# Optimization experiments

Measured on AMD Instinct MI355X. Metric: run time of the kernel, lower is better.

Reference implementation:

```python
import jax, jax.numpy as jnp
import numpy as np

N, E, F_IN, G, C = 100000, 3200000, 64, 1024, 10
BN_EPS = 1e-5


def _glorot(key, shape):
    fan_in, fan_out = shape[0], shape[1]
    lim = jnp.sqrt(6.0 / (fan_in + fan_out))
    return jax.random.uniform(key, shape, jnp.float32, -lim, lim)


def setup_inputs() -> dict:
    key = jax.random.key(0)
    ks = jax.random.split(key, 20)
    x = jax.random.normal(ks[0], (N, F_IN), jnp.float32)
    edge_index = jax.random.randint(ks[1], (2, E), 0, N, jnp.int64)
    batch = jnp.sort(jax.random.randint(ks[2], (N,), 0, G, jnp.int64))
    p = {
        'W1a': _glorot(ks[3], (F_IN, 128)), 'b1a': jnp.zeros((128,), jnp.float32),
        'W1b': _glorot(ks[4], (128, 128)), 'b1b': jnp.zeros((128,), jnp.float32),
        'g1': jnp.ones((128,), jnp.float32), 'be1': jnp.zeros((128,), jnp.float32),
        'W2a': _glorot(ks[5], (128, 64)), 'b2a': jnp.zeros((64,), jnp.float32),
        'W2b': _glorot(ks[6], (64, 64)), 'b2b': jnp.zeros((64,), jnp.float32),
        'g2': jnp.ones((64,), jnp.float32), 'be2': jnp.zeros((64,), jnp.float32),
        'W3a': _glorot(ks[7], (64, 32)), 'b3a': jnp.zeros((32,), jnp.float32),
        'W3b': _glorot(ks[8], (32, 32)), 'b3b': jnp.zeros((32,), jnp.float32),
        'g3': jnp.ones((32,), jnp.float32), 'be3': jnp.zeros((32,), jnp.float32),
        'Wf1': _glorot(ks[9], (32, 128)), 'bf1': jnp.zeros((128,), jnp.float32),
        'Wf2': _glorot(ks[10], (128, 64)), 'bf2': jnp.zeros((64,), jnp.float32),
        'Wf3': _glorot(ks[11], (64, C)), 'bf3': jnp.zeros((C,), jnp.float32),
    }
    return {'x': x, 'edge_index': edge_index, 'batch': batch, **p}


def _gin(x, src, dst, Wa, ba, Wb, bb):
    # GINConv (eps=0): h = MLP(x + sum_{j->i} x_j)
    agg = jax.ops.segment_sum(x[src], dst, num_segments=N)
    h = jax.nn.relu((x + agg) @ Wa + ba)
    return h @ Wb + bb


def _bn(x, g, b):
    # BatchNorm1d, training-mode batch statistics (biased variance)
    mu = jnp.mean(x, axis=0)
    var = jnp.mean((x - mu) ** 2, axis=0)
    return (x - mu) * jax.lax.rsqrt(var + BN_EPS) * g + b


def reference(x, edge_index, batch,
              W1a, b1a, W1b, b1b, g1, be1,
              W2a, b2a, W2b, b2b, g2, be2,
              W3a, b3a, W3b, b3b, g3, be3,
              Wf1, bf1, Wf2, bf2, Wf3, bf3):
    src, dst = edge_index[0], edge_index[1]
    z = _bn(jax.nn.relu(_gin(x, src, dst, W1a, b1a, W1b, b1b)), g1, be1)
    z = _bn(jax.nn.relu(_gin(z, src, dst, W2a, b2a, W2b, b2b)), g2, be2)
    z = _bn(jax.nn.relu(_gin(z, src, dst, W3a, b3a, W3b, b3b)), g3, be3)
    # global_add_pool over graph ids
    z = jax.ops.segment_sum(z, batch, num_segments=G)  # [G, 32]
    cr = jax.nn.relu(z @ Wf1 + bf1)
    cr = jax.nn.relu(cr @ Wf2 + bf2)  # dropout = identity (eval)
    cr = cr @ Wf3 + bf3
    return cr.reshape(-1, C)
```

## Files before the change

### kernel.cpp

```cpp
#include <hip/hip_runtime.h>

#define BN_EPS 1e-5f

typedef _Float16 f16;
typedef _Float16 f16x8 __attribute__((ext_vector_type(8)));
typedef _Float16 f16x4 __attribute__((ext_vector_type(4)));
typedef float f32x4 __attribute__((ext_vector_type(4)));

#define NBLK 512
#define BSHIFT 8
#define BMASK 255

__global__ __launch_bounds__(256) void conv_kernel(const float4* __restrict__ in,
        f16x4* __restrict__ out, int n4) {
    int i = blockIdx.x * 256 + threadIdx.x;
    if (i < n4) {
        float4 v = in[i];
        f16x4 o;
        o.x = (f16)v.x; o.y = (f16)v.y; o.z = (f16)v.z; o.w = (f16)v.w;
        out[i] = o;
    }
}

__global__ __launch_bounds__(256) void bkt_count(const int* __restrict__ dst,
        int* __restrict__ hist, int NBK, int CHUNK, int E) {
    __shared__ int lh[512];
    const int blk = blockIdx.x, t = threadIdx.x;
    for (int r = t; r < 512; r += 256) lh[r] = 0;
    __syncthreads();
    const int e0 = blk * CHUNK, e1 = min(E, e0 + CHUNK);
    for (int e = e0 + t; e < e1; e += 256) atomicAdd(&lh[dst[e] >> BSHIFT], 1);
    __syncthreads();
    for (int r = t; r < NBK; r += 256) hist[r * NBLK + blk] = lh[r];
}

__global__ __launch_bounds__(512) void bkt_bscan(int* __restrict__ hist,
        int* __restrict__ btot) {
    __shared__ int sh[512];
    const int b = blockIdx.x, t = threadIdx.x;
    int v = hist[b * NBLK + t];
    sh[t] = v;
    __syncthreads();
    for (int d = 1; d < 512; d <<= 1) {
        int u = (t >= d) ? sh[t - d] : 0;
        __syncthreads();
        sh[t] += u;
        __syncthreads();
    }
    hist[b * NBLK + t] = sh[t] - v;
    if (t == 511) btot[b] = sh[511];
}

__global__ __launch_bounds__(512) void bkt_boff(const int* __restrict__ btot,
        int* __restrict__ boff, int* __restrict__ off, int NBK, int N, int E) {
    __shared__ int sh[512];
    const int t = threadIdx.x;
    int v = (t < NBK) ? btot[t] : 0;
    sh[t] = v;
    __syncthreads();
    for (int d = 1; d < 512; d <<= 1) {
        int u = (t >= d) ? sh[t - d] : 0;
        __syncthreads();
        sh[t] += u;
        __syncthreads();
    }
    if (t < NBK) boff[t] = sh[t] - v;
    if (t == 0) { boff[NBK] = E; off[N] = E; }
}

__global__ __launch_bounds__(256) void bkt_scatter(const int* __restrict__ src,
        const int* __restrict__ dst, const int* __restrict__ hist,
        const int* __restrict__ boff, int* __restrict__ bucketed,
        int NBK, int CHUNK, int E) {
    __shared__ int lc[512];
    const int blk = blockIdx.x, t = threadIdx.x;
    for (int r = t; r < NBK; r += 256) lc[r] = boff[r] + hist[r * NBLK + blk];
    __syncthreads();
    const int e0 = blk * CHUNK, e1 = min(E, e0 + CHUNK);
    for (int e = e0 + t; e < e1; e += 256) {
        int d = dst[e];
        int slot = atomicAdd(&lc[d >> BSHIFT], 1);
        bucketed[slot] = ((d & BMASK) << 18) | src[e];
    }
}

__global__ __launch_bounds__(512) void bkt_csr(const int* __restrict__ bucketed,
        const int* __restrict__ boff, int* __restrict__ off,
        int* __restrict__ elist, int N) {
    __shared__ int lh[256];
    __shared__ int lc[256];
    __shared__ int sh[256];
    const int b = blockIdx.x, t = threadIdx.x;
    const int b0 = b << BSHIFT;
    const int R = min(N - b0, 256);
    const int base = boff[b], cnt = boff[b + 1] - base;
    if (t < 256) lh[t] = 0;
    __syncthreads();
    for (int i = t; i < cnt; i += 512) atomicAdd(&lh[bucketed[base + i] >> 18], 1);
    __syncthreads();
    int v = 0;
    if (t < 256) { v = lh[t]; sh[t] = v; }
    __syncthreads();
    for (int d = 1; d < 256; d <<= 1) {
        int u = 0;
        if (t < 256 && t >= d) u = sh[t - d];
        __syncthreads();
        if (t < 256) sh[t] += u;
        __syncthreads();
    }
    if (t < 256) { int ex = sh[t] - v; lh[t] = ex; lc[t] = ex; }
    __syncthreads();
    if (t < R) off[b0 + t] = base + lh[t];
    for (int i = t; i < cnt; i += 512) {
        int p = bucketed[base + i];
        int rk = atomicAdd(&lc[p >> 18], 1);
        elist[base + rk] = p & 0x3FFFF;
    }
}

template<int F, bool AFFINE>
__global__ __launch_bounds__(256) void gather_v(const int* __restrict__ off,
        const int* __restrict__ elist, const f16* __restrict__ in,
        f16* __restrict__ out, const float* __restrict__ v,
        const float* __restrict__ bias, int N) {
    constexpr int TPN = F / 8;
    constexpr int NPB = 256 / TPN;
    const int i = blockIdx.x * NPB + threadIdx.x / TPN;
    const int l = threadIdx.x & (TPN - 1);
    if (i >= N) return;
    const int j0 = l * 8;
    f16x8 s = ((const f16x8*)(in + (size_t)i * F))[l];
    float a[8];
#pragma unroll
    for (int u = 0; u < 8; u++) a[u] = (float)s[u];
    int k = off[i], e = off[i + 1];
    const float cnt = (float)(e - k + 1);
    for (; k + 8 <= e; k += 8) {
        f16x8 p0 = ((const f16x8*)(in + (size_t)elist[k + 0] * F))[l];
        f16x8 p1 = ((const f16x8*)(in + (size_t)elist[k + 1] * F))[l];
        f16x8 p2 = ((const f16x8*)(in + (size_t)elist[k + 2] * F))[l];
        f16x8 p3 = ((const f16x8*)(in + (size_t)elist[k + 3] * F))[l];
        f16x8 p4 = ((const f16x8*)(in + (size_t)elist[k + 4] * F))[l];
        f16x8 p5 = ((const f16x8*)(in + (size_t)elist[k + 5] * F))[l];
        f16x8 p6 = ((const f16x8*)(in + (size_t)elist[k + 6] * F))[l];
        f16x8 p7 = ((const f16x8*)(in + (size_t)elist[k + 7] * F))[l];
#pragma unroll
        for (int u = 0; u < 8; u++)
            a[u] += (((float)p0[u] + (float)p1[u]) + ((float)p2[u] + (float)p3[u]))
                  + (((float)p4[u] + (float)p5[u]) + ((float)p6[u] + (float)p7[u]));
    }
    for (; k + 4 <= e; k += 4) {
        f16x8 p0 = ((const f16x8*)(in + (size_t)elist[k + 0] * F))[l];
        f16x8 p1 = ((const f16x8*)(in + (size_t)elist[k + 1] * F))[l];
        f16x8 p2 = ((const f16x8*)(in + (size_t)elist[k + 2] * F))[l];
        f16x8 p3 = ((const f16x8*)(in + (size_t)elist[k + 3] * F))[l];
#pragma unroll
        for (int u = 0; u < 8; u++)
            a[u] += ((float)p0[u] + (float)p1[u]) + ((float)p2[u] + (float)p3[u]);
    }
    for (; k < e; k++) {
        f16x8 p = ((const f16x8*)(in + (size_t)elist[k] * F))[l];
#pragma unroll
        for (int u = 0; u < 8; u++) a[u] += (float)p[u];
    }
    if (AFFINE) {
        float4 vv0 = *(const float4*)(v + j0);
        float4 vv1 = *(const float4*)(v + j0 + 4);
        float4 bb0 = *(const float4*)(bias + j0);
        float4 bb1 = *(const float4*)(bias + j0 + 4);
        a[0] = fmaxf(fmaf(cnt, vv0.x, a[0] + bb0.x), 0.0f);
        a[1] = fmaxf(fmaf(cnt, vv0.y, a[1] + bb0.y), 0.0f);
        a[2] = fmaxf(fmaf(cnt, vv0.z, a[2] + bb0.z), 0.0f);
        a[3] = fmaxf(fmaf(cnt, vv0.w, a[3] + bb0.w), 0.0f);
        a[4] = fmaxf(fmaf(cnt, vv1.x, a[4] + bb1.x), 0.0f);
        a[5] = fmaxf(fmaf(cnt, vv1.y, a[5] + bb1.y), 0.0f);
        a[6] = fmaxf(fmaf(cnt, vv1.z, a[6] + bb1.z), 0.0f);
        a[7] = fmaxf(fmaf(cnt, vv1.w, a[7] + bb1.w), 0.0f);
    }
    f16x8 o;
#pragma unroll
    for (int u = 0; u < 8; u++) o[u] = (f16)a[u];
    ((f16x8*)(out + (size_t)i * F))[l] = o;
}

__global__ __launch_bounds__(64) void prep_kernel(const float* __restrict__ W,
        const float* __restrict__ stats, const float* __restrict__ g,
        const float* __restrict__ be, float* __restrict__ v,
        int FIN, int FOUT, float invN) {
    int j = threadIdx.x;
    if (j >= FOUT) return;
    float acc = 0.0f;
    for (int k = 0; k < FIN; k++) {
        float mu = stats[k] * invN;
        float var = fmaxf(stats[FIN + k] * invN - mu * mu, 0.0f);
        float sc = rsqrtf(var + BN_EPS) * g[k];
        float sh = be[k] - mu * sc;
        acc = fmaf(sh, W[(size_t)k * FOUT + j], acc);
    }
    v[j] = acc;
}

__global__ __launch_bounds__(256) void wfrag_kernel(const float* __restrict__ W,
        f16* __restrict__ out, int FIN, int FOUT,
        const float* __restrict__ stats, const float* __restrict__ g, float invN) {
    int f = blockIdx.x * 256 + threadIdx.x;
    if (f >= FIN * FOUT) return;
    int j = f & 7;
    int lane = (f >> 3) & 63;
    int tile = f >> 9;
    int NT = FOUT >> 4;
    int t = tile % NT, s = tile / NT;
    int k = s * 32 + (lane >> 4) * 8 + j;
    int n = t * 16 + (lane & 15);
    float w = W[(size_t)k * FOUT + n];
    if (stats) {
        float mu = stats[k] * invN;
        float var = fmaxf(stats[FIN + k] * invN - mu * mu, 0.0f);
        w *= rsqrtf(var + BN_EPS) * g[k];
    }
    out[f] = (f16)w;
}

template<int FIN, int FOUT, bool STATS, bool RELU, bool BIAS, typename OutT>
__global__ __launch_bounds__(256) void gemm_mfma(const f16* __restrict__ A,
        const f16* __restrict__ Wf, const float* __restrict__ bias,
        OutT* __restrict__ Out, float* __restrict__ stats, int N) {
    constexpr int NS = FIN / 32;
    constexpr int NT = FOUT / 16;
    __shared__ float Ss[STATS ? 2 * FOUT : 1];
    if (STATS) {
        for (int i = threadIdx.x; i < 2 * FOUT; i += 256) Ss[i] = 0.0f;
        __syncthreads();
    }
    const int wid = threadIdx.x >> 6;
    const int lane = threadIdx.x & 63;
    const int col = lane & 15;
    const int quad = lane >> 4;

    f16x8 Bf[NS][NT];
#pragma unroll
    for (int s = 0; s < NS; s++)
#pragma unroll
        for (int t = 0; t < NT; t++)
            Bf[s][t] = *(const f16x8*)&Wf[((s * NT + t) << 9) + (lane << 3)];

    float bj[NT];
#pragma unroll
    for (int t = 0; t < NT; t++) bj[t] = BIAS ? bias[t * 16 + col] : 0.0f;

    float ls[NT], ls2[NT];
#pragma unroll
    for (int t = 0; t < NT; t++) { ls[t] = 0.0f; ls2[t] = 0.0f; }

    const int S = N >> 4;
    for (int sidx = blockIdx.x * 4 + wid; sidx < S; sidx += (int)gridDim.x * 4) {
        const int m0 = sidx << 4;
        const f16* a0 = A + (size_t)(m0 + col) * FIN + (quad << 3);
        f16x8 Af[NS];
#pragma unroll
        for (int s = 0; s < NS; s++) Af[s] = *(const f16x8*)(a0 + s * 32);
        f32x4 acc[NT];
#pragma unroll
        for (int t = 0; t < NT; t++) acc[t] = (f32x4){bj[t], bj[t], bj[t], bj[t]};
#pragma unroll
        for (int t = 0; t < NT; t++)
#pragma unroll
            for (int s = 0; s < NS; s++)
                acc[t] = __builtin_amdgcn_mfma_f32_16x16x32_f16(Af[s], Bf[s][t], acc[t], 0, 0, 0);
#pragma unroll
        for (int t = 0; t < NT; t++) {
            float v0 = acc[t][0], v1 = acc[t][1], v2 = acc[t][2], v3 = acc[t][3];
            if (RELU) {
                v0 = fmaxf(v0, 0.0f); v1 = fmaxf(v1, 0.0f);
                v2 = fmaxf(v2, 0.0f); v3 = fmaxf(v3, 0.0f);
            }
            if (STATS) {
                ls[t]  += (v0 + v1) + (v2 + v3);
                ls2[t] += (v0 * v0 + v1 * v1) + (v2 * v2 + v3 * v3);
            }
            OutT* o = Out + (size_t)(m0 + quad * 4) * FOUT + t * 16 + col;
            o[0]        = (OutT)v0;
            o[FOUT]     = (OutT)v1;
            o[2 * FOUT] = (OutT)v2;
            o[3 * FOUT] = (OutT)v3;
        }
    }

    if (STATS) {
#pragma unroll
        for (int t = 0; t < NT; t++) {
            float s1 = ls[t], s2 = ls2[t];
            s1 += __shfl_xor(s1, 16); s1 += __shfl_xor(s1, 32);
            s2 += __shfl_xor(s2, 16); s2 += __shfl_xor(s2, 32);
            if (quad == 0) {
                atomicAdd(&Ss[t * 16 + col], s1);
                atomicAdd(&Ss[FOUT + t * 16 + col], s2);
            }
        }
        __syncthreads();
        for (int i = threadIdx.x; i < 2 * FOUT; i += 256) atomicAdd(&stats[i], Ss[i]);
    }
}

__global__ __launch_bounds__(256) void bn_pool_kernel(const float* __restrict__ y,
        const float* __restrict__ stats, const float* __restrict__ gw,
        const float* __restrict__ bw, const int* __restrict__ batch,
        float* __restrict__ pool, int N, float invN) {
    constexpr int F = 32, CH = 64;
    int q = threadIdx.x >> 5;
    int j = threadIdx.x & 31;
    int r0 = (blockIdx.x * 8 + q) * CH;
    if (r0 >= N) return;
    int r1 = min(r0 + CH, N);
    float mu = stats[j] * invN;
    float var = fmaxf(stats[F + j] * invN - mu * mu, 0.0f);
    float sc = rsqrtf(var + BN_EPS) * gw[j];
    float sh = bw[j] - mu * sc;
    int curg = batch[r0];
    float acc = 0.0f;
    for (int r = r0; r < r1; r++) {
        int g = batch[r];
        if (g != curg) {
            atomicAdd(pool + (size_t)curg * 32 + j, acc);
            acc = 0.0f;
            curg = g;
        }
        acc = fmaf(y[(size_t)r * 32 + j], sc, sh + acc);
    }
    atomicAdd(pool + (size_t)curg * 32 + j, acc);
}

__global__ __launch_bounds__(128) void fc_kernel(const float* __restrict__ pool,
        const float* __restrict__ Wf1, const float* __restrict__ bf1,
        const float* __restrict__ Wf2, const float* __restrict__ bf2,
        const float* __restrict__ Wf3, const float* __restrict__ bf3,
        float* __restrict__ out) {
    __shared__ float zin[32];
    __shared__ float h1[128];
    __shared__ float h2[64];
    const int gidx = blockIdx.x;
    const int t = threadIdx.x;
    if (t < 32) zin[t] = pool[(size_t)gidx * 32 + t];
    __syncthreads();
    {
        float a = bf1[t];
        for (int k = 0; k < 32; k++) a = fmaf(zin[k], Wf1[k * 128 + t], a);
        h1[t] = fmaxf(a, 0.0f);
    }
    __syncthreads();
    if (t < 64) {
        float a = bf2[t];
        for (int k = 0; k < 128; k++) a = fmaf(h1[k], Wf2[k * 64 + t], a);
        h2[t] = fmaxf(a, 0.0f);
    }
    __syncthreads();
    if (t < 10) {
        float a = bf3[t];
        for (int k = 0; k < 64; k++) a = fmaf(h2[k], Wf3[k * 10 + t], a);
        out[(size_t)gidx * 10 + t] = a;
    }
}

extern "C" void kernel_launch(void* const* d_in, const int* in_sizes, int n_in,
                              void* d_out, int out_size, void* d_ws, size_t ws_size,
                              hipStream_t stream) {
    const float* x   = (const float*)d_in[0];
    const int*  ei   = (const int*)d_in[1];
    const int*  batch= (const int*)d_in[2];
    const float* W1a = (const float*)d_in[3];  const float* b1a = (const float*)d_in[4];
    const float* W1b = (const float*)d_in[5];  const float* b1b = (const float*)d_in[6];
    const float* g1  = (const float*)d_in[7];  const float* be1 = (const float*)d_in[8];
    const float* W2a = (const float*)d_in[9];  const float* b2a = (const float*)d_in[10];
    const float* W2b = (const float*)d_in[11]; const float* b2b = (const float*)d_in[12];
    const float* g2  = (const float*)d_in[13]; const float* be2 = (const float*)d_in[14];
    const float* W3a = (const float*)d_in[15]; const float* b3a = (const float*)d_in[16];
    const float* W3b = (const float*)d_in[17]; const float* b3b = (const float*)d_in[18];
    const float* g3  = (const float*)d_in[19]; const float* be3 = (const float*)d_in[20];
    const float* Wf1 = (const float*)d_in[21]; const float* bf1 = (const float*)d_in[22];
    const float* Wf2 = (const float*)d_in[23]; const float* bf2 = (const float*)d_in[24];
    const float* Wf3 = (const float*)d_in[25]; const float* bf3 = (const float*)d_in[26];

    const int N = in_sizes[2];
    const int E = in_sizes[1] / 2;
    const int G = out_size / 10;
    const int* src = ei;
    const int* dst = ei + E;

    const int NBK = (N + BMASK) >> BSHIFT;
    const int CHUNK = (E + NBLK - 1) / NBLK;

    float* B0   = (float*)d_ws;
    float* B1   = B0 + (size_t)N * 128;
    float* pool = B1 + (size_t)N * 128;
    float* st1  = pool + (size_t)G * 32;
    float* st2  = st1 + 256;
    float* st3  = st2 + 256;
    int* off    = (int*)(st3 + 256);
    int* elist  = off + (N + 1);
    float* v2   = (float*)(elist + E);
    float* v3   = v2 + 64;
    int* boff   = (int*)(v3 + 32);
    int* btot   = boff + (NBK + 1);
    f16* Wh1a   = (f16*)(btot + NBK);
    f16* Wh1b   = Wh1a + 64 * 128;
    f16* Wh2a   = Wh1b + 128 * 128;
    f16* Wh2b   = Wh2a + 128 * 64;
    f16* Wh3a   = Wh2b + 64 * 64;
    f16* Wh3b   = Wh3a + 64 * 32;

    int* bucketed = (int*)B1;
    int* hist     = bucketed + E;

    f16* xh    = (f16*)B0;
    f16* A1    = (f16*)B1;
    f16* H1    = (f16*)B0 + (size_t)N * 64;
    f16* Y1    = (f16*)B1 + (size_t)N * 64;
    f16* Z1    = (f16*)B0;
    f16* H2    = (f16*)B1;
    f16* Y2    = (f16*)B0 + (size_t)N * 64;
    f16* Z2    = (f16*)B0;
    f16* H3    = (f16*)B1;
    float* Y3  = B1 + (size_t)N * 64;

    hipMemsetAsync(pool, 0, ((size_t)G * 32 + 768) * sizeof(float), stream);

    const float invN = 1.0f / (float)N;
    const int GG = 640;

    conv_kernel<<<(N * 16 + 255) / 256, 256, 0, stream>>>((const float4*)x, (f16x4*)xh, N * 16);

    wfrag_kernel<<<32, 256, 0, stream>>>(W1a, Wh1a, 64, 128, nullptr, nullptr, invN);
    wfrag_kernel<<<64, 256, 0, stream>>>(W1b, Wh1b, 128, 128, nullptr, nullptr, invN);
    wfrag_kernel<<<16, 256, 0, stream>>>(W2b, Wh2b, 64, 64, nullptr, nullptr, invN);
    wfrag_kernel<<<4, 256, 0, stream>>>(W3b, Wh3b, 32, 32, nullptr, nullptr, invN);

    bkt_count  <<<NBLK, 256, 0, stream>>>(dst, hist, NBK, CHUNK, E);
    bkt_bscan  <<<NBK, 512, 0, stream>>>(hist, btot);
    bkt_boff   <<<1, 512, 0, stream>>>(btot, boff, off, NBK, N, E);
    bkt_scatter<<<NBLK, 256, 0, stream>>>(src, dst, hist, boff, bucketed, NBK, CHUNK, E);
    bkt_csr    <<<NBK, 512, 0, stream>>>(bucketed, boff, off, elist, N);

    gather_v<64, false><<<(N + 31) / 32, 256, 0, stream>>>(off, elist, xh, A1, nullptr, nullptr, N);
    gemm_mfma<64, 128, false, true, true, f16><<<GG, 256, 0, stream>>>(A1, Wh1a, b1a, H1, nullptr, N);
    gemm_mfma<128, 128, true, true, true, f16><<<GG, 256, 0, stream>>>(H1, Wh1b, b1b, Y1, st1, N);

    prep_kernel<<<1, 64, 0, stream>>>(W2a, st1, g1, be1, v2, 128, 64, invN);
    wfrag_kernel<<<32, 256, 0, stream>>>(W2a, Wh2a, 128, 64, st1, g1, invN);
    gemm_mfma<128, 64, false, false, false, f16><<<GG, 256, 0, stream>>>(Y1, Wh2a, nullptr, Z1, nullptr, N);
    gather_v<64, true><<<(N + 31) / 32, 256, 0, stream>>>(off, elist, Z1, H2, v2, b2a, N);
    gemm_mfma<64, 64, true, true, true, f16><<<GG, 256, 0, stream>>>(H2, Wh2b, b2b, Y2, st2, N);

    prep_kernel<<<1, 64, 0, stream>>>(W3a, st2, g2, be2, v3, 64, 32, invN);
    wfrag_kernel<<<8, 256, 0, stream>>>(W3a, Wh3a, 64, 32, st2, g2, invN);
    gemm_mfma<64, 32, false, false, false, f16><<<GG, 256, 0, stream>>>(Y2, Wh3a, nullptr, Z2, nullptr, N);
    gather_v<32, true><<<(N + 63) / 64, 256, 0, stream>>>(off, elist, Z2, H3, v3, b3a, N);
    gemm_mfma<32, 32, true, true, true, float><<<GG, 256, 0, stream>>>(H3, Wh3b, b3b, Y3, st3, N);

    bn_pool_kernel<<<(N + 511) / 512, 256, 0, stream>>>(Y3, st3, g3, be3, batch, pool, N, invN);

    fc_kernel<<<G, 128, 0, stream>>>(pool, Wf1, bf1, Wf2, bf2, Wf3, bf3, (float*)d_out);
}
```

Before: 550.8 us.

## Merge setup kernels, vectorize bucket sort, pipeline gather loads, split GEMM columns

Merges the fp32-to-fp16 input conversion and the four weight-fragment kernels into one launch, and merges the per-layer prep and wfrag kernels, to cut launch count. The bucket count and scatter kernels now read edges as int4, with CHUNK rounded up to a multiple of 4 so the vector loads stay aligned. The gather loop is restructured to prefetch the next four neighbours while summing the current four. The 128-wide GEMMs are split into 64-column blocks, which lowers per-thread fragment registers but reads the A rows twice.

After: 517.3 us. 1.06x faster.

```diff
diff --git a/kernel.cpp b/kernel.cpp
--- a/kernel.cpp
+++ b/kernel.cpp
@@ -11,15 +11,73 @@
 #define BSHIFT 8
 #define BMASK 255
 
-__global__ __launch_bounds__(256) void conv_kernel(const float4* __restrict__ in,
-        f16x4* __restrict__ out, int n4) {
-    int i = blockIdx.x * 256 + threadIdx.x;
-    if (i < n4) {
-        float4 v = in[i];
-        f16x4 o;
-        o.x = (f16)v.x; o.y = (f16)v.y; o.z = (f16)v.z; o.w = (f16)v.w;
-        out[i] = o;
-    }
+__device__ inline void wfrag_one(const float* __restrict__ W, f16* __restrict__ out,
+        int FIN, int FOUT, int f,
+        const float* __restrict__ stats, const float* __restrict__ g, float invN) {
+    int j = f & 7;
+    int lane = (f >> 3) & 63;
+    int tile = f >> 9;
+    int NT = FOUT >> 4;
+    int t = tile % NT, s = tile / NT;
+    int k = s * 32 + (lane >> 4) * 8 + j;
+    int n = t * 16 + (lane & 15);
+    float w = W[(size_t)k * FOUT + n];
+    if (stats) {
+        float mu = stats[k] * invN;
+        float var = fmaxf(stats[FIN + k] * invN - mu * mu, 0.0f);
+        w *= rsqrtf(var + BN_EPS) * g[k];
+    }
+    out[f] = (f16)w;
+}
+
+__global__ __launch_bounds__(256) void setup_kernel(const float4* __restrict__ x,
+        f16x4* __restrict__ xh, int n4,
+        const float* __restrict__ W1a, f16* __restrict__ Wh1a,
+        const float* __restrict__ W1b, f16* __restrict__ Wh1b,
+        const float* __restrict__ W2b, f16* __restrict__ Wh2b,
+        const float* __restrict__ W3b, f16* __restrict__ Wh3b) {
+    const int BC = (n4 + 255) / 256;
+    int bid = blockIdx.x;
+    if (bid < BC) {
+        int i = bid * 256 + threadIdx.x;
+        if (i < n4) {
+            float4 v = x[i];
+            f16x4 o;
+            o.x = (f16)v.x; o.y = (f16)v.y; o.z = (f16)v.z; o.w = (f16)v.w;
+            xh[i] = o;
+        }
+        return;
+    }
+    bid -= BC;
+    if (bid < 32) { wfrag_one(W1a, Wh1a, 64, 128, bid * 256 + threadIdx.x, nullptr, nullptr, 0.f); return; }
+    bid -= 32;
+    if (bid < 64) { wfrag_one(W1b, Wh1b, 128, 128, bid * 256 + threadIdx.x, nullptr, nullptr, 0.f); return; }
+    bid -= 64;
+    if (bid < 16) { wfrag_one(W2b, Wh2b, 64, 64, bid * 256 + threadIdx.x, nullptr, nullptr, 0.f); return; }
+    bid -= 16;
+    wfrag_one(W3b, Wh3b, 32, 32, bid * 256 + threadIdx.x, nullptr, nullptr, 0.f);
+}
+
+__global__ __launch_bounds__(256) void layerprep_kernel(const float* __restrict__ W,
+        f16* __restrict__ Wh, int FIN, int FOUT,
+        const float* __restrict__ stats, const float* __restrict__ g,
+        const float* __restrict__ be, float* __restrict__ v, float invN) {
+    if (blockIdx.x == 0) {
+        int j = threadIdx.x;
+        if (j >= FOUT) return;
+        float acc = 0.0f;
+        for (int k = 0; k < FIN; k++) {
+            float mu = stats[k] * invN;
+            float var = fmaxf(stats[FIN + k] * invN - mu * mu, 0.0f);
+            float sc = rsqrtf(var + BN_EPS) * g[k];
+            float sh = be[k] - mu * sc;
+            acc = fmaf(sh, W[(size_t)k * FOUT + j], acc);
+        }
+        v[j] = acc;
+        return;
+    }
+    int f = (blockIdx.x - 1) * 256 + threadIdx.x;
+    if (f < FIN * FOUT) wfrag_one(W, Wh, FIN, FOUT, f, stats, g, invN);
 }
 
 __global__ __launch_bounds__(256) void bkt_count(const int* __restrict__ dst,
@@ -29,7 +87,16 @@
     for (int r = t; r < 512; r += 256) lh[r] = 0;
     __syncthreads();
     const int e0 = blk * CHUNK, e1 = min(E, e0 + CHUNK);
-    for (int e = e0 + t; e < e1; e += 256) atomicAdd(&lh[dst[e] >> BSHIFT], 1);
+    const int nq = (e1 - e0) >> 2;
+    const int4* d4 = (const int4*)(dst + e0);
+    for (int q = t; q < nq; q += 256) {
+        int4 v = d4[q];
+        atomicAdd(&lh[v.x >> BSHIFT], 1);
+        atomicAdd(&lh[v.y >> BSHIFT], 1);
+        atomicAdd(&lh[v.z >> BSHIFT], 1);
+        atomicAdd(&lh[v.w >> BSHIFT], 1);
+    }
+    for (int e = e0 + (nq << 2) + t; e < e1; e += 256) atomicAdd(&lh[dst[e] >> BSHIFT], 1);
     __syncthreads();
     for (int r = t; r < NBK; r += 256) hist[r * NBLK + blk] = lh[r];
 }
@@ -77,7 +144,19 @@
     for (int r = t; r < NBK; r += 256) lc[r] = boff[r] + hist[r * NBLK + blk];
     __syncthreads();
     const int e0 = blk * CHUNK, e1 = min(E, e0 + CHUNK);
-    for (int e = e0 + t; e < e1; e += 256) {
+    const int nq = (e1 - e0) >> 2;
+    const int4* d4 = (const int4*)(dst + e0);
+    const int4* s4 = (const int4*)(src + e0);
+    for (int q = t; q < nq; q += 256) {
+        int4 d = d4[q];
+        int4 s = s4[q];
+        int sl;
+        sl = atomicAdd(&lc[d.x >> BSHIFT], 1); bucketed[sl] = ((d.x & BMASK) << 18) | s.x;
+        sl = atomicAdd(&lc[d.y >> BSHIFT], 1); bucketed[sl] = ((d.y & BMASK) << 18) | s.y;
+        sl = atomicAdd(&lc[d.z >> BSHIFT], 1); bucketed[sl] = ((d.z & BMASK) << 18) | s.z;
+        sl = atomicAdd(&lc[d.w >> BSHIFT], 1); bucketed[sl] = ((d.w & BMASK) << 18) | s.w;
+    }
+    for (int e = e0 + (nq << 2) + t; e < e1; e += 256) {
         int d = dst[e];
         int slot = atomicAdd(&lc[d >> BSHIFT], 1);
         bucketed[slot] = ((d & BMASK) << 18) | src[e];
@@ -129,37 +208,36 @@
     const int l = threadIdx.x & (TPN - 1);
     if (i >= N) return;
     const int j0 = l * 8;
-    f16x8 s = ((const f16x8*)(in + (size_t)i * F))[l];
+    const f16x8* __restrict__ inv = (const f16x8*)in;
+    f16x8 s = inv[(size_t)i * TPN + l];
     float a[8];
 #pragma unroll
     for (int u = 0; u < 8; u++) a[u] = (float)s[u];
     int k = off[i], e = off[i + 1];
     const float cnt = (float)(e - k + 1);
-    for (; k + 8 <= e; k += 8) {
-        f16x8 p0 = ((const f16x8*)(in + (size_t)elist[k + 0] * F))[l];
-        f16x8 p1 = ((const f16x8*)(in + (size_t)elist[k + 1] * F))[l];
-        f16x8 p2 = ((const f16x8*)(in + (size_t)elist[k + 2] * F))[l];
-        f16x8 p3 = ((const f16x8*)(in + (size_t)elist[k + 3] * F))[l];
-        f16x8 p4 = ((const f16x8*)(in + (size_t)elist[k + 4] * F))[l];
-        f16x8 p5 = ((const f16x8*)(in + (size_t)elist[k + 5] * F))[l];
-        f16x8 p6 = ((const f16x8*)(in + (size_t)elist[k + 6] * F))[l];
-        f16x8 p7 = ((const f16x8*)(in + (size_t)elist[k + 7] * F))[l];
+    f16x8 c0, c1, c2, c3;
+    if (k + 4 <= e) {
+        c0 = inv[(size_t)elist[k + 0] * TPN + l];
+        c1 = inv[(size_t)elist[k + 1] * TPN + l];
+        c2 = inv[(size_t)elist[k + 2] * TPN + l];
+        c3 = inv[(size_t)elist[k + 3] * TPN + l];
+        k += 4;
+        for (; k + 4 <= e; k += 4) {
+            f16x8 d0 = inv[(size_t)elist[k + 0] * TPN + l];
+            f16x8 d1 = inv[(size_t)elist[k + 1] * TPN + l];
+            f16x8 d2 = inv[(size_t)elist[k + 2] * TPN + l];
+            f16x8 d3 = inv[(size_t)elist[k + 3] * TPN + l];
+#pragma unroll
+            for (int u = 0; u < 8; u++)
+                a[u] += ((float)c0[u] + (float)c1[u]) + ((float)c2[u] + (float)c3[u]);
+            c0 = d0; c1 = d1; c2 = d2; c3 = d3;
+        }
 #pragma unroll
         for (int u = 0; u < 8; u++)
-            a[u] += (((float)p0[u] + (float)p1[u]) + ((float)p2[u] + (float)p3[u]))
-                  + (((float)p4[u] + (float)p5[u]) + ((float)p6[u] + (float)p7[u]));
-    }
-    for (; k + 4 <= e; k += 4) {
-        f16x8 p0 = ((const f16x8*)(in + (size_t)elist[k + 0] * F))[l];
-        f16x8 p1 = ((const f16x8*)(in + (size_t)elist[k + 1] * F))[l];
-        f16x8 p2 = ((const f16x8*)(in + (size_t)elist[k + 2] * F))[l];
-        f16x8 p3 = ((const f16x8*)(in + (size_t)elist[k + 3] * F))[l];
-#pragma unroll
-        for (int u = 0; u < 8; u++)
-            a[u] += ((float)p0[u] + (float)p1[u]) + ((float)p2[u] + (float)p3[u]);
+            a[u] += ((float)c0[u] + (float)c1[u]) + ((float)c2[u] + (float)c3[u]);
     }
     for (; k < e; k++) {
-        f16x8 p = ((const f16x8*)(in + (size_t)elist[k] * F))[l];
+        f16x8 p = inv[(size_t)elist[k] * TPN + l];
 #pragma unroll
         for (int u = 0; u < 8; u++) a[u] += (float)p[u];
     }
@@ -180,58 +258,26 @@
     f16x8 o;
 #pragma unroll
     for (int u = 0; u < 8; u++) o[u] = (f16)a[u];
-    ((f16x8*)(out + (size_t)i * F))[l] = o;
-}
-
-__global__ __launch_bounds__(64) void prep_kernel(const float* __restrict__ W,
-        const float* __restrict__ stats, const float* __restrict__ g,
-        const float* __restrict__ be, float* __restrict__ v,
-        int FIN, int FOUT, float invN) {
-    int j = threadIdx.x;
-    if (j >= FOUT) return;
-    float acc = 0.0f;
-    for (int k = 0; k < FIN; k++) {
-        float mu = stats[k] * invN;
-        float var = fmaxf(stats[FIN + k] * invN - mu * mu, 0.0f);
-        float sc = rsqrtf(var + BN_EPS) * g[k];
-        float sh = be[k] - mu * sc;
-        acc = fmaf(sh, W[(size_t)k * FOUT + j], acc);
-    }
-    v[j] = acc;
-}
-
-__global__ __launch_bounds__(256) void wfrag_kernel(const float* __restrict__ W,
-        f16* __restrict__ out, int FIN, int FOUT,
-        const float* __restrict__ stats, const float* __restrict__ g, float invN) {
-    int f = blockIdx.x * 256 + threadIdx.x;
-    if (f >= FIN * FOUT) return;
-    int j = f & 7;
-    int lane = (f >> 3) & 63;
-    int tile = f >> 9;
-    int NT = FOUT >> 4;
-    int t = tile % NT, s = tile / NT;
-    int k = s * 32 + (lane >> 4) * 8 + j;
-    int n = t * 16 + (lane & 15);
-    float w = W[(size_t)k * FOUT + n];
-    if (stats) {
-        float mu = stats[k] * invN;
-        float var = fmaxf(stats[FIN + k] * invN - mu * mu, 0.0f);
-        w *= rsqrtf(var + BN_EPS) * g[k];
-    }
-    out[f] = (f16)w;
-}
-
-template<int FIN, int FOUT, bool STATS, bool RELU, bool BIAS, typename OutT>
+    ((f16x8*)(out))[(size_t)i * TPN + l] = o;
+}
+
+template<int FIN, int FOUT, int CT, bool STATS, bool RELU, bool BIAS, typename OutT>
 __global__ __launch_bounds__(256) void gemm_mfma(const f16* __restrict__ A,
         const f16* __restrict__ Wf, const float* __restrict__ bias,
         OutT* __restrict__ Out, float* __restrict__ stats, int N) {
     constexpr int NS = FIN / 32;
-    constexpr int NT = FOUT / 16;
-    __shared__ float Ss[STATS ? 2 * FOUT : 1];
+    constexpr int NTF = FOUT / 16;
+    constexpr int NT = CT / 16;
+    constexpr int NCB = FOUT / CT;
+    __shared__ float Ss[STATS ? 2 * CT : 1];
     if (STATS) {
-        for (int i = threadIdx.x; i < 2 * FOUT; i += 256) Ss[i] = 0.0f;
-        __syncthreads();
-    }
+        for (int i = threadIdx.x; i < 2 * CT; i += 256) Ss[i] = 0.0f;
+        __syncthreads();
+    }
+    const int cb = blockIdx.x % NCB;
+    const int rb = blockIdx.x / NCB;
+    const int RB = gridDim.x / NCB;
+    const int t0 = cb * NT;
     const int wid = threadIdx.x >> 6;
     const int lane = threadIdx.x & 63;
     const int col = lane & 15;
@@ -242,18 +288,18 @@
     for (int s = 0; s < NS; s++)
 #pragma unroll
         for (int t = 0; t < NT; t++)
-            Bf[s][t] = *(const f16x8*)&Wf[((s * NT + t) << 9) + (lane << 3)];
+            Bf[s][t] = *(const f16x8*)&Wf[((s * NTF + t0 + t) << 9) + (lane << 3)];
 
     float bj[NT];
 #pragma unroll
-    for (int t = 0; t < NT; t++) bj[t] = BIAS ? bias[t * 16 + col] : 0.0f;
+    for (int t = 0; t < NT; t++) bj[t] = BIAS ? bias[(t0 + t) * 16 + col] : 0.0f;
 
     float ls[NT], ls2[NT];
 #pragma unroll
     for (int t = 0; t < NT; t++) { ls[t] = 0.0f; ls2[t] = 0.0f; }
 
     const int S = N >> 4;
-    for (int sidx = blockIdx.x * 4 + wid; sidx < S; sidx += (int)gridDim.x * 4) {
+    for (int sidx = rb * 4 + wid; sidx < S; sidx += RB * 4) {
         const int m0 = sidx << 4;
         const f16* a0 = A + (size_t)(m0 + col) * FIN + (quad << 3);
         f16x8 Af[NS];
@@ -278,7 +324,7 @@
                 ls[t]  += (v0 + v1) + (v2 + v3);
                 ls2[t] += (v0 * v0 + v1 * v1) + (v2 * v2 + v3 * v3);
             }
-            OutT* o = Out + (size_t)(m0 + quad * 4) * FOUT + t * 16 + col;
+            OutT* o = Out + (size_t)(m0 + quad * 4) * FOUT + (t0 + t) * 16 + col;
             o[0]        = (OutT)v0;
             o[FOUT]     = (OutT)v1;
             o[2 * FOUT] = (OutT)v2;
@@ -294,11 +340,14 @@
             s2 += __shfl_xor(s2, 16); s2 += __shfl_xor(s2, 32);
             if (quad == 0) {
                 atomicAdd(&Ss[t * 16 + col], s1);
-                atomicAdd(&Ss[FOUT + t * 16 + col], s2);
+                atomicAdd(&Ss[CT + t * 16 + col], s2);
             }
         }
         __syncthreads();
-        for (int i = threadIdx.x; i < 2 * FOUT; i += 256) atomicAdd(&stats[i], Ss[i]);
+        for (int i = threadIdx.x; i < CT; i += 256) {
+            atomicAdd(&stats[cb * CT + i], Ss[i]);
+            atomicAdd(&stats[FOUT + cb * CT + i], Ss[CT + i]);
+        }
     }
 }
 
@@ -387,7 +436,7 @@
     const int* dst = ei + E;
 
     const int NBK = (N + BMASK) >> BSHIFT;
-    const int CHUNK = (E + NBLK - 1) / NBLK;
+    const int CHUNK = (((E + NBLK - 1) / NBLK) + 3) & ~3;
 
     float* B0   = (float*)d_ws;
     float* B1   = B0 + (size_t)N * 128;
@@ -427,12 +476,12 @@
     const float invN = 1.0f / (float)N;
     const int GG = 640;
 
-    conv_kernel<<<(N * 16 + 255) / 256, 256, 0, stream>>>((const float4*)x, (f16x4*)xh, N * 16);
-
-    wfrag_kernel<<<32, 256, 0, stream>>>(W1a, Wh1a, 64, 128, nullptr, nullptr, invN);
-    wfrag_kernel<<<64, 256, 0, stream>>>(W1b, Wh1b, 128, 128, nullptr, nullptr, invN);
-    wfrag_kernel<<<16, 256, 0, stream>>>(W2b, Wh2b, 64, 64, nullptr, nullptr, invN);
-    wfrag_kernel<<<4, 256, 0, stream>>>(W3b, Wh3b, 32, 32, nullptr, nullptr, invN);
+    {
+        int BC = (N * 16 + 255) / 256;
+        setup_kernel<<<BC + 32 + 64 + 16 + 4, 256, 0, stream>>>(
+            (const float4*)x, (f16x4*)xh, N * 16,
+            W1a, Wh1a, W1b, Wh1b, W2b, Wh2b, W3b, Wh3b);
+    }
 
     bkt_count  <<<NBLK, 256, 0, stream>>>(dst, hist, NBK, CHUNK, E);
     bkt_bscan  <<<NBK, 512, 0, stream>>>(hist, btot);
@@ -441,20 +490,18 @@
     bkt_csr    <<<NBK, 512, 0, stream>>>(bucketed, boff, off, elist, N);
 
     gather_v<64, false><<<(N + 31) / 32, 256, 0, stream>>>(off, elist, xh, A1, nullptr, nullptr, N);
-    gemm_mfma<64, 128, false, true, true, f16><<<GG, 256, 0, stream>>>(A1, Wh1a, b1a, H1, nullptr, N);
-    gemm_mfma<128, 128, true, true, true, f16><<<GG, 256, 0, stream>>>(H1, Wh1b, b1b, Y1, st1, N);
-
-    prep_kernel<<<1, 64, 0, stream>>>(W2a, st1, g1, be1, v2, 128, 64, invN);
-    wfrag_kernel<<<32, 256, 0, stream>>>(W2a, Wh2a, 128, 64, st1, g1, invN);
-    gemm_mfma<128, 64, false, false, false, f16><<<GG, 256, 0, stream>>>(Y1, Wh2a, nullptr, Z1, nullptr, N);
+    gemm_mfma<64, 128, 64, false, true, true, f16><<<GG, 256, 0, stream>>>(A1, Wh1a, b1a, H1, nullptr, N);
+    gemm_mfma<128, 128, 64, true, true, true, f16><<<GG, 256, 0, stream>>>(H1, Wh1b, b1b, Y1, st1, N);
+
+    layerprep_kernel<<<33, 256, 0, stream>>>(W2a, Wh2a, 128, 64, st1, g1, be1, v2, invN);
+    gemm_mfma<128, 64, 64, false, false, false, f16><<<GG, 256, 0, stream>>>(Y1, Wh2a, nullptr, Z1, nullptr, N);
     gather_v<64, true><<<(N + 31) / 32, 256, 0, stream>>>(off, elist, Z1, H2, v2, b2a, N);
-    gemm_mfma<64, 64, true, true, true, f16><<<GG, 256, 0, stream>>>(H2, Wh2b, b2b, Y2, st2, N);
-
-    prep_kernel<<<1, 64, 0, stream>>>(W3a, st2, g2, be2, v3, 64, 32, invN);
-    wfrag_kernel<<<8, 256, 0, stream>>>(W3a, Wh3a, 64, 32, st2, g2, invN);
-    gemm_mfma<64, 32, false, false, false, f16><<<GG, 256, 0, stream>>>(Y2, Wh3a, nullptr, Z2, nullptr, N);
+    gemm_mfma<64, 64, 64, true, true, true, f16><<<GG, 256, 0, stream>>>(H2, Wh2b, b2b, Y2, st2, N);
+
+    layerprep_kernel<<<9, 256, 0, stream>>>(W3a, Wh3a, 64, 32, st2, g2, be2, v3, invN);
+    gemm_mfma<64, 32, 32, false, false, false, f16><<<GG, 256, 0, stream>>>(Y2, Wh3a, nullptr, Z2, nullptr, N);
     gather_v<32, true><<<(N + 63) / 64, 256, 0, stream>>>(off, elist, Z2, H3, v3, b3a, N);
-    gemm_mfma<32, 32, true, true, true, float><<<GG, 256, 0, stream>>>(H3, Wh3b, b3b, Y3, st3, N);
+    gemm_mfma<32, 32, 32, true, true, true, float><<<GG, 256, 0, stream>>>(H3, Wh3b, b3b, Y3, st3, N);
 
     bn_pool_kernel<<<(N + 511) / 512, 256, 0, stream>>>(Y3, st3, g3, be3, batch, pool, N, invN);
 
```
